# Optimization experiments

Measured on AMD Instinct MI355X. Metric: run time of the kernel, lower is better.

Reference implementation:

```python
import jax, jax.numpy as jnp
import numpy as np

VF = 3          # vote_factor
GRID = 0.1      # grid_size
P = 4           # padded per-group capacity (stands in for data-dependent max group size)
RATIO_MAX = 5   # original drops groups needing repeat ratio > 5
EPS = 1e-5
SHIFT, BASE = 512, 1024  # 3D->1D hash (int32-safe: BASE**3 < 2**31)


def _bn_relu(x, gamma, beta):
    # BatchNorm1d in train mode over the token (batch) axis; conv input is (N, C, 1)
    m = x.mean(axis=0)
    v = jnp.mean((x - m) ** 2, axis=0)  # biased variance, as torch BN uses for normalization
    return jax.nn.relu((x - m) * jax.lax.rsqrt(v + EPS) * gamma + beta)


def _one_sample(idv, cov, ftv, W1, b1, g1, be1, W2, b2, g2, be2, W3, b3):
    N, C = ftv.shape
    V = N * VF
    # conv1x1 stack == per-token linear layers
    h = _bn_relu(ftv @ W1.T + b1, g1, be1)
    h = _bn_relu(h @ W2.T + b2, g2, be2)
    log = (h @ W3.T + b3).reshape(N, VF, 3 + C)
    off3 = log[:, :, :3]                                  # (N, VF, 3)
    coor = (cov[:, None, :] + off3).reshape(V, 3)
    grid_res = (off3 / GRID).astype(jnp.int32)            # trunc toward zero, like .int()
    ind = (idv[:, None, :] + grid_res).reshape(V, 3)
    # Degenerate inner-dict loop (tensor keys hash by identity): every vote's feature
    # offset becomes offset[n][VF-1] * 3 / VF  (len(key)==3, idx stale at VF-1)
    feat_off = log[:, VF - 1, 3:] * (3.0 / VF)            # (N, C)
    feat = jnp.broadcast_to((ftv + feat_off)[:, None, :], (N, VF, C)).reshape(V, C)

    # group votes by quantized 3D index (tuple-key dict -> hash + unique + segment ops)
    hc = jnp.clip(ind, -SHIFT, SHIFT - 1) + SHIFT
    keys = (hc[:, 0] * BASE + hc[:, 1]) * BASE + hc[:, 2]  # (V,) int32
    _, inv = jnp.unique(keys, size=V, fill_value=-1, return_inverse=True)
    inv = inv.reshape(-1)
    ones = jnp.ones((V,), jnp.int32)
    counts = jax.ops.segment_sum(ones, inv, num_segments=V)          # group sizes
    order = jnp.argsort(inv)                                          # votes sorted by group
    starts = jnp.cumsum(counts) - counts
    first = jax.ops.segment_min(jnp.arange(V, dtype=jnp.int32), inv, num_segments=V)
    first = jnp.where(counts > 0, first, 0)
    ind_buf = jnp.where((counts > 0)[:, None], ind[first], 0).astype(jnp.int32)

    cnt_safe = jnp.maximum(counts, 1)
    p = jnp.arange(P, dtype=jnp.int32)
    src_pos = starts[:, None] + (p[None, :] % cnt_safe[:, None])      # (V, P) repeat-fill
    src = order[src_pos]
    valid = (counts > 0) & (counts * RATIO_MAX >= P)                  # ceil(P/cnt) <= 5
    coor_buf = jnp.where(valid[:, None, None], coor[src], 0.0)        # (V, P, 3)
    feat_buf = jnp.where(valid[:, None, None], feat[src], 0.0)        # (V, P, C)
    return ind_buf, coor_buf, feat_buf, valid


def setup_inputs() -> dict:
    key = jax.random.key(0)
    ks = jax.random.split(key, 12)
    B, N, C = 2, 16384, 128
    s = 1.0 / np.sqrt(C)
    return {
        "ID": jax.random.randint(ks[0], (B, N, 3), 0, 100, dtype=jnp.int32),
        "CO": jax.random.normal(ks[1], (B, N, 3), jnp.float32),
        "FT": jax.random.normal(ks[2], (B, N, C), jnp.float32),
        "W1": jax.random.normal(ks[3], (C, C), jnp.float32) * s,
        "b1": jnp.zeros((C,), jnp.float32),
        "g1": 1.0 + 0.1 * jax.random.normal(ks[4], (C,), jnp.float32),
        "be1": 0.1 * jax.random.normal(ks[5], (C,), jnp.float32),
        "W2": jax.random.normal(ks[6], (C, C), jnp.float32) * s,
        "b2": jnp.zeros((C,), jnp.float32),
        "g2": 1.0 + 0.1 * jax.random.normal(ks[7], (C,), jnp.float32),
        "be2": 0.1 * jax.random.normal(ks[8], (C,), jnp.float32),
        "W3": jax.random.normal(ks[9], ((3 + C) * VF, C), jnp.float32) * s,
        "b3": 0.01 * jax.random.normal(ks[10], ((3 + C) * VF,), jnp.float32),
    }


def reference(ID, CO, FT, W1, b1, g1, be1, W2, b2, g2, be2, W3, b3):
    outs = [_one_sample(ID[i], CO[i], FT[i], W1, b1, g1, be1, W2, b2, g2, be2, W3, b3)
            for i in range(ID.shape[0])]  # small fixed batch loop
    ind_buf = jnp.stack([o[0] for o in outs])
    coor_buf = jnp.stack([o[1] for o in outs])
    feat_buf = jnp.stack([o[2] for o in outs])
    mask = jnp.stack([o[3] for o in outs])
    return ind_buf, coor_buf, feat_buf, mask
```

## Files before the change

### kernel.cpp

```cpp
#include <hip/hip_runtime.h>

constexpr int Bn = 2;
constexpr int Nn = 16384;
constexpr int Cc = 128;
constexpr int Vv = Nn * 3;
constexpr int Pp = 4;
constexpr int SB = 48;
constexpr int HB = 96;

constexpr size_t IND0  = 0;
constexpr size_t COOR0 = (size_t)Bn * Vv * 3;
constexpr size_t FEAT0 = COOR0 + (size_t)Bn * Vv * Pp * 3;
constexpr size_t MASK0 = FEAT0 + (size_t)Bn * Vv * Pp * Cc;

__global__ __launch_bounds__(256) void gemm1(
    const float* __restrict__ A, const float* __restrict__ W,
    const float* __restrict__ bias, float* __restrict__ out,
    unsigned* __restrict__ HZ)
{
    __shared__ float As[64 * 36];
    __shared__ float Ws[128 * 36];

    int t = threadIdx.x;
    {
        int gid = blockIdx.x * 256 + t;
        if (gid < 3 * Bn * SB * 1024 / 4)
            ((uint4*)HZ)[gid] = make_uint4(0u, 0u, 0u, 0u);
    }

    int bid = blockIdx.x;
    int s = bid >> 8, rb = bid & 255;
    const float* Ag = A + (size_t)s * Nn * Cc + (size_t)rb * 64 * Cc;
    float* outg = out + (size_t)s * Nn * Cc + (size_t)rb * 64 * Cc;

    int tx = t & 15, ty = t >> 4;
    int arow = t >> 3, ac4 = (t & 7) * 4;

    float acc[4][8];
    #pragma unroll
    for (int i = 0; i < 4; ++i)
        #pragma unroll
        for (int j = 0; j < 8; ++j) acc[i][j] = 0.f;

    float4 aR[2], wR[4];
    #pragma unroll
    for (int r = 0; r < 2; ++r)
        aR[r] = *(const float4*)(Ag + (size_t)(arow + r * 32) * Cc + ac4);
    #pragma unroll
    for (int r = 0; r < 4; ++r)
        wR[r] = *(const float4*)(W + (size_t)(arow + r * 32) * Cc + ac4);

    for (int stage = 0; stage < 4; ++stage) {
        if (stage) __syncthreads();
        #pragma unroll
        for (int r = 0; r < 2; ++r)
            *(float4*)&As[(arow + r * 32) * 36 + ac4] = aR[r];
        #pragma unroll
        for (int r = 0; r < 4; ++r)
            *(float4*)&Ws[(arow + r * 32) * 36 + ac4] = wR[r];
        if (stage < 3) {
            int k1 = (stage + 1) * 32;
            #pragma unroll
            for (int r = 0; r < 2; ++r)
                aR[r] = *(const float4*)(Ag + (size_t)(arow + r * 32) * Cc + k1 + ac4);
            #pragma unroll
            for (int r = 0; r < 4; ++r)
                wR[r] = *(const float4*)(W + (size_t)(arow + r * 32) * Cc + k1 + ac4);
        }
        __syncthreads();
        #pragma unroll
        for (int k4 = 0; k4 < 8; ++k4) {
            int k = k4 * 4;
            float4 av[4];
            #pragma unroll
            for (int i = 0; i < 4; ++i) av[i] = *(const float4*)&As[(i * 16 + ty) * 36 + k];
            #pragma unroll
            for (int j = 0; j < 8; ++j) {
                float4 wv = *(const float4*)&Ws[(j * 16 + tx) * 36 + k];
                #pragma unroll
                for (int i = 0; i < 4; ++i) {
                    float a0 = acc[i][j];
                    a0 = fmaf(av[i].x, wv.x, a0);
                    a0 = fmaf(av[i].y, wv.y, a0);
                    a0 = fmaf(av[i].z, wv.z, a0);
                    a0 = fmaf(av[i].w, wv.w, a0);
                    acc[i][j] = a0;
                }
            }
        }
    }
    #pragma unroll
    for (int j = 0; j < 8; ++j) {
        int col = j * 16 + tx;
        float bv = bias[col];
        #pragma unroll
        for (int i = 0; i < 4; ++i)
            outg[(size_t)(i * 16 + ty) * Cc + col] = acc[i][j] + bv;
    }
}

__global__ __launch_bounds__(256) void gemm_t2(
    const float* __restrict__ A, const float* __restrict__ W,
    const float* __restrict__ bias, const float* __restrict__ part,
    const float* __restrict__ g, const float* __restrict__ be,
    float* __restrict__ out)
{
    __shared__ float As[64 * 36];
    __shared__ float Ws[128 * 36];
    __shared__ float ssl[2 * Cc];

    int t = threadIdx.x;
    int bid = blockIdx.x;
    int s = bid >> 8, rb = bid & 255;
    const float* Ag = A + (size_t)s * Nn * Cc + (size_t)rb * 64 * Cc;
    float* outg = out + (size_t)s * Nn * Cc + (size_t)rb * 64 * Cc;

    if (t < Cc) {
        const float* pp = part + (size_t)s * 64 * 2 * Cc;
        float sm = 0.f, sq = 0.f;
        #pragma unroll 8
        for (int b = 0; b < 64; ++b) {
            sm += pp[(size_t)b * 2 * Cc + t];
            sq += pp[(size_t)b * 2 * Cc + Cc + t];
        }
        float m   = sm / (float)Nn;
        float var = sq / (float)Nn - m * m;
        float inv = 1.0f / sqrtf(var + 1e-5f);
        float sc  = g[t] * inv;
        ssl[t]      = sc;
        ssl[Cc + t] = be[t] - m * sc;
    }
    __syncthreads();

    int tx = t & 15, ty = t >> 4;
    int arow = t >> 3, ac4 = (t & 7) * 4;

    float acc[4][8];
    #pragma unroll
    for (int i = 0; i < 4; ++i)
        #pragma unroll
        for (int j = 0; j < 8; ++j) acc[i][j] = 0.f;

    float4 aR[2], wR[4];
    #pragma unroll
    for (int r = 0; r < 2; ++r)
        aR[r] = *(const float4*)(Ag + (size_t)(arow + r * 32) * Cc + ac4);
    #pragma unroll
    for (int r = 0; r < 4; ++r)
        wR[r] = *(const float4*)(W + (size_t)(arow + r * 32) * Cc + ac4);

    for (int stage = 0; stage < 4; ++stage) {
        int k0 = stage * 32;
        if (stage) __syncthreads();
        #pragma unroll
        for (int r = 0; r < 2; ++r) {
            float4 v = aR[r];
            int ch = k0 + ac4;
            v.x = fmaxf(0.f, fmaf(v.x, ssl[ch + 0], ssl[Cc + ch + 0]));
            v.y = fmaxf(0.f, fmaf(v.y, ssl[ch + 1], ssl[Cc + ch + 1]));
            v.z = fmaxf(0.f, fmaf(v.z, ssl[ch + 2], ssl[Cc + ch + 2]));
            v.w = fmaxf(0.f, fmaf(v.w, ssl[ch + 3], ssl[Cc + ch + 3]));
            *(float4*)&As[(arow + r * 32) * 36 + ac4] = v;
        }
        #pragma unroll
        for (int r = 0; r < 4; ++r)
            *(float4*)&Ws[(arow + r * 32) * 36 + ac4] = wR[r];
        if (stage < 3) {
            int k1 = k0 + 32;
            #pragma unroll
            for (int r = 0; r < 2; ++r)
                aR[r] = *(const float4*)(Ag + (size_t)(arow + r * 32) * Cc + k1 + ac4);
            #pragma unroll
            for (int r = 0; r < 4; ++r)
                wR[r] = *(const float4*)(W + (size_t)(arow + r * 32) * Cc + k1 + ac4);
        }
        __syncthreads();
        #pragma unroll
        for (int k4 = 0; k4 < 8; ++k4) {
            int k = k4 * 4;
            float4 av[4];
            #pragma unroll
            for (int i = 0; i < 4; ++i) av[i] = *(const float4*)&As[(i * 16 + ty) * 36 + k];
            #pragma unroll
            for (int j = 0; j < 8; ++j) {
                float4 wv = *(const float4*)&Ws[(j * 16 + tx) * 36 + k];
                #pragma unroll
                for (int i = 0; i < 4; ++i) {
                    float a0 = acc[i][j];
                    a0 = fmaf(av[i].x, wv.x, a0);
                    a0 = fmaf(av[i].y, wv.y, a0);
                    a0 = fmaf(av[i].z, wv.z, a0);
                    a0 = fmaf(av[i].w, wv.w, a0);
                    acc[i][j] = a0;
                }
            }
        }
    }
    #pragma unroll
    for (int j = 0; j < 8; ++j) {
        int col = j * 16 + tx;
        float bv = bias[col];
        #pragma unroll
        for (int i = 0; i < 4; ++i)
            outg[(size_t)(i * 16 + ty) * Cc + col] = acc[i][j] + bv;
    }
}

__global__ __launch_bounds__(256) void gemm3_fused(
    const float* __restrict__ A, const float* __restrict__ W,
    const float* __restrict__ bias, const float* __restrict__ part,
    const float* __restrict__ g, const float* __restrict__ be,
    const float* __restrict__ FT, const float* __restrict__ CO,
    const int* __restrict__ ID,
    float* __restrict__ featb, float* __restrict__ coor,
    int* __restrict__ indb, unsigned* __restrict__ keys,
    unsigned* __restrict__ idx0, unsigned* __restrict__ hist0)
{
    __shared__ float As[64 * 36];
    __shared__ float Ws[144 * 36];
    __shared__ float ssl[2 * Cc];

    int bid = blockIdx.x;
    int s = bid >> 8, rb = bid & 255;
    const float* Ag = A + (size_t)s * Nn * Cc + (size_t)rb * 64 * Cc;

    int t = threadIdx.x, tx = t & 15, ty = t >> 4;

    if (t < Cc) {
        const float* pp = part + (size_t)s * 64 * 2 * Cc;
        float sm = 0.f, sq = 0.f;
        #pragma unroll 8
        for (int b = 0; b < 64; ++b) {
            sm += pp[(size_t)b * 2 * Cc + t];
            sq += pp[(size_t)b * 2 * Cc + Cc + t];
        }
        float m   = sm / (float)Nn;
        float var = sq / (float)Nn - m * m;
        float inv = 1.0f / sqrtf(var + 1e-5f);
        float sc  = g[t] * inv;
        ssl[t]      = sc;
        ssl[Cc + t] = be[t] - m * sc;
    }
    __syncthreads();

    float acc[4][9];
    #pragma unroll
    for (int i = 0; i < 4; ++i)
        #pragma unroll
        for (int j = 0; j < 9; ++j) acc[i][j] = 0.f;

    for (int stage = 0; stage < 4; ++stage) {
        int k0 = stage * 32;
        if (stage) __syncthreads();
        #pragma unroll
        for (int r = 0; r < 2; ++r) {
            int idx = r * 256 + t;
            int row = idx >> 3, c4 = (idx & 7) * 4;
            float4 v = *(const float4*)(Ag + (size_t)row * Cc + k0 + c4);
            int ch = k0 + c4;
            v.x = fmaxf(0.f, fmaf(v.x, ssl[ch + 0], ssl[Cc + ch + 0]));
            v.y = fmaxf(0.f, fmaf(v.y, ssl[ch + 1], ssl[Cc + ch + 1]));
            v.z = fmaxf(0.f, fmaf(v.z, ssl[ch + 2], ssl[Cc + ch + 2]));
            v.w = fmaxf(0.f, fmaf(v.w, ssl[ch + 3], ssl[Cc + ch + 3]));
            *(float4*)&As[row * 36 + c4] = v;
        }
        for (int idx = t; idx < 144 * 8; idx += 256) {
            int row = idx >> 3, c4 = (idx & 7) * 4;
            float4 v = make_float4(0.f, 0.f, 0.f, 0.f);
            if (row < 137) {
                int wr = (row < 9) ? (row / 3) * 131 + (row % 3) : row + 256;
                v = *(const float4*)(W + (size_t)wr * Cc + k0 + c4);
            }
            *(float4*)&Ws[row * 36 + c4] = v;
        }
        __syncthreads();
        #pragma unroll
        for (int k4 = 0; k4 < 8; ++k4) {
            int k = k4 * 4;
            float4 av[4];
            #pragma unroll
            for (int i = 0; i < 4; ++i) av[i] = *(const float4*)&As[(i * 16 + ty) * 36 + k];
            #pragma unroll
            for (int j = 0; j < 9; ++j) {
                float4 wv = *(const float4*)&Ws[(j * 16 + tx) * 36 + k];
                #pragma unroll
                for (int i = 0; i < 4; ++i) {
                    float a0 = acc[i][j];
                    a0 = fmaf(av[i].x, wv.x, a0);
                    a0 = fmaf(av[i].y, wv.y, a0);
                    a0 = fmaf(av[i].z, wv.z, a0);
                    a0 = fmaf(av[i].w, wv.w, a0);
                    acc[i][j] = a0;
                }
            }
        }
    }

    __syncthreads();
    __shared__ float L9[64 * 12];
    int n0 = rb * 64;
    const float* FTg = FT + ((size_t)s * Nn + n0) * Cc;
    float* FBg = featb + ((size_t)s * Nn + n0) * Cc;
    #pragma unroll
    for (int j = 0; j < 9; ++j) {
        int col = j * 16 + tx;
        if (col < 9) {
            float bv = bias[(col / 3) * 131 + col % 3];
            #pragma unroll
            for (int i = 0; i < 4; ++i)
                L9[(i * 16 + ty) * 12 + col] = acc[i][j] + bv;
        } else if (col < 137) {
            int ch = col - 9;
            float bv = bias[col + 256];
            #pragma unroll
            for (int i = 0; i < 4; ++i) {
                int row = i * 16 + ty;
                float lg = acc[i][j] + bv;
                FBg[(size_t)row * Cc + ch] = FTg[(size_t)row * Cc + ch] + lg;
            }
        }
    }
    __syncthreads();
    if (t < 192) {
        int row = t / 3, jv = t - row * 3;
        int n = n0 + row, v = n * 3 + jv;
        size_t vb = (size_t)s * Vv + v;
        float o0 = L9[row * 12 + jv * 3 + 0];
        float o1 = L9[row * 12 + jv * 3 + 1];
        float o2 = L9[row * 12 + jv * 3 + 2];
        const float* co = CO + ((size_t)s * Nn + n) * 3;
        coor[vb * 3 + 0] = co[0] + o0;
        coor[vb * 3 + 1] = co[1] + o1;
        coor[vb * 3 + 2] = co[2] + o2;
        const int* id = ID + ((size_t)s * Nn + n) * 3;
        int gi0 = (int)(o0 / 0.1f), gi1 = (int)(o1 / 0.1f), gi2 = (int)(o2 / 0.1f);
        int i0 = id[0] + gi0, i1 = id[1] + gi1, i2 = id[2] + gi2;
        indb[vb * 3 + 0] = i0; indb[vb * 3 + 1] = i1; indb[vb * 3 + 2] = i2;
        int h0 = min(max(i0, -512), 511) + 512;
        int h1 = min(max(i1, -512), 511) + 512;
        int h2 = min(max(i2, -512), 511) + 512;
        unsigned key = ((unsigned)h0 * 1024u + (unsigned)h1) * 1024u + (unsigned)h2;
        keys[vb] = key;
        idx0[vb] = (unsigned)v;
        atomicAdd(&hist0[(size_t)s * SB * 1024 + (size_t)(v >> 10) * 1024 + (key & 1023u)], 1u);
    }
}

__global__ void colstats(const float* __restrict__ Y, float* __restrict__ part)
{
    int blk = blockIdx.x;
    int s = blk >> 6, b = blk & 63;
    const float* Yp = Y + (size_t)s * Nn * Cc + (size_t)b * 256 * Cc;
    int c = threadIdx.x;
    float sm = 0.f, sq = 0.f;
    #pragma unroll 8
    for (int r = 0; r < 256; ++r) {
        float v = Yp[(size_t)r * Cc + c];
        sm += v; sq += v * v;
    }
    float* pp = part + ((size_t)s * 64 + b) * 2 * Cc;
    pp[c] = sm;
    pp[Cc + c] = sq;
}

template<int PASS>
__global__ __launch_bounds__(512) void scat(
    const unsigned* __restrict__ kIn, const unsigned* __restrict__ iIn,
    unsigned* __restrict__ kOut, unsigned* __restrict__ iOut,
    const unsigned* __restrict__ hist, unsigned* __restrict__ nextH)
{
    __shared__ unsigned hw[8 * 1024];
    __shared__ unsigned tot[1024];
    __shared__ unsigned wtot[8];
    int t = threadIdx.x, lane = t & 63, w = t >> 6;
    int blk = blockIdx.x, s = blk / SB, b = blk % SB;

    #pragma unroll
    for (int i = 0; i < 16; ++i) hw[w * 1024 + i * 64 + lane] = 0u;

    const uint2* hs2 = (const uint2*)(hist + (size_t)s * SB * 1024);
    int d0 = 2 * t, d1 = 2 * t + 1;
    unsigned run0 = 0, run1 = 0, my0 = 0, my1 = 0;
    #pragma unroll 4
    for (int bb = 0; bb < SB; ++bb) {
        uint2 v = hs2[bb * 512 + t];
        if (bb == b) { my0 = run0; my1 = run1; }
        run0 += v.x; run1 += v.y;
    }
    unsigned pair = run0 + run1;
    unsigned S = pair;
    #pragma unroll
    for (int o = 1; o < 64; o <<= 1) {
        unsigned v = __shfl_up(S, o);
        if (lane >= o) S += v;
    }
    unsigned pairExcl = S - pair;
    unsigned wTot = __shfl(S, 63);
    if (lane == 63) wtot[w] = S;
    __syncthreads();
    unsigned waveBase = 0;
    #pragma unroll
    for (int ww = 0; ww < 8; ++ww)
        if (ww < w) waveBase += wtot[ww];
    (void)wTot;
    tot[d0] = waveBase + pairExcl + my0;
    tot[d1] = waveBase + pairExcl + run0 + my1;

    size_t base = (size_t)s * Vv + (size_t)b * 1024;
    unsigned keyE[2], idxE[2], rkE[2], dE[2];
    #pragma unroll
    for (int e = 0; e < 2; ++e) {
        int pos = w * 128 + e * 64 + lane;
        keyE[e] = kIn[base + pos];
        idxE[e] = iIn[base + pos];
        unsigned d = (keyE[e] >> (PASS * 10)) & 1023u;
        dE[e] = d;
        unsigned long long m = ~0ull;
        #pragma unroll
        for (int bit = 0; bit < 10; ++bit) {
            bool bbit = (d >> bit) & 1u;
            unsigned long long bal = __ballot(bbit);
            m &= bbit ? bal : ~bal;
        }
        int lanesBelow = __popcll(m & ((1ull << lane) - 1ull));
        int cnt = __popcll(m);
        int leader = __ffsll((unsigned long long)m) - 1;
        unsigned basec = hw[w * 1024 + d];
        if (lane == leader) hw[w * 1024 + d] = basec + (unsigned)cnt;
        rkE[e] = basec + (unsigned)lanesBelow;
    }
    __syncthreads();
    {
        unsigned r0 = 0, r1 = 0;
        for (int ww = 0; ww < 8; ++ww) {
            unsigned v0 = hw[ww * 1024 + d0], v1 = hw[ww * 1024 + d1];
            hw[ww * 1024 + d0] = r0; hw[ww * 1024 + d1] = r1;
            r0 += v0; r1 += v1;
        }
    }
    __syncthreads();
    #pragma unroll
    for (int e = 0; e < 2; ++e) {
        unsigned dest = tot[dE[e]] + hw[w * 1024 + dE[e]] + rkE[e];
        kOut[(size_t)s * Vv + dest] = keyE[e];
        iOut[(size_t)s * Vv + dest] = idxE[e];
        if constexpr (PASS < 2) {
            unsigned d2 = (keyE[e] >> ((PASS + 1) * 10)) & 1023u;
            atomicAdd(&nextH[(size_t)s * SB * 1024 + (size_t)(dest >> 10) * 1024 + d2], 1u);
        }
    }
}

__global__ __launch_bounds__(512) void ranksall(const unsigned* __restrict__ skeys,
                                                unsigned* __restrict__ start,
                                                unsigned* __restrict__ nu)
{
    int blk = blockIdx.x;
    int s = blk / HB, cb = blk % HB;
    int t = threadIdx.x, lane = t & 63, w = t >> 6;
    size_t base = (size_t)s * Vv;

    __shared__ unsigned cnt[HB];
    __shared__ unsigned pre[HB + 1];
    __shared__ unsigned wsum[8];

    for (int cc = w * 12; cc < w * 12 + 12; ++cc) {
        unsigned tc = 0;
        #pragma unroll
        for (int sub = 0; sub < 8; ++sub) {
            int i = cc * 512 + sub * 64 + lane;
            unsigned k = skeys[base + i];
            bool head = (i == 0) || (skeys[base + i - 1] != k);
            tc += (unsigned)__popcll(__ballot(head));
        }
        if (lane == 0) cnt[cc] = tc;
    }
    __syncthreads();
    if (t == 0) {
        unsigned run = 0;
        for (int i = 0; i < HB; ++i) { pre[i] = run; run += cnt[i]; }
        pre[HB] = run;
    }
    __syncthreads();

    int i = cb * 512 + t;
    unsigned k = skeys[base + i];
    bool head = (i == 0) || (skeys[base + i - 1] != k);
    unsigned long long bal = __ballot(head);
    if (lane == 0) wsum[w] = (unsigned)__popcll(bal);
    __syncthreads();
    unsigned wbase = 0;
    for (int ww = 0; ww < w; ++ww) wbase += wsum[ww];
    unsigned lpre = (unsigned)__popcll(bal & ((1ull << lane) - 1ull));
    if (head)
        start[(size_t)s * (Vv + 1) + pre[cb] + wbase + lpre] = (unsigned)i;
    if (cb == 0 && t == 0) {
        nu[s] = pre[HB];
        start[(size_t)s * (Vv + 1) + pre[HB]] = (unsigned)Vv;
    }
}

__global__ __launch_bounds__(512) void outputk(
    const unsigned* __restrict__ sidx, const unsigned* __restrict__ start,
    const unsigned* __restrict__ nu, const int* __restrict__ indb,
    const float* __restrict__ coor, const float* __restrict__ featb,
    float* __restrict__ out)
{
    int wid = threadIdx.x >> 6, lane = threadIdx.x & 63;
    int g = blockIdx.x * 8 + wid;
    int s = g / Vv, u = g - s * Vv;
    size_t su = (size_t)s * Vv + u;
    bool valid = (unsigned)u < nu[s];
    float4* out4 = (float4*)out;
    int f = lane & 31, jlo = lane >> 5;
    if (valid) {
        const unsigned* st = start + (size_t)s * (Vv + 1);
        unsigned i0 = st[u], i1 = st[u + 1];
        unsigned c = i1 - i0;
        unsigned my = sidx[(size_t)s * Vv + i0 + ((unsigned)(lane & 3)) % c];
        unsigned sv[4];
        sv[0] = __shfl(my, 0); sv[1] = __shfl(my, 1);
        sv[2] = __shfl(my, 2); sv[3] = __shfl(my, 3);
        const float4* fb = (const float4*)(featb + (size_t)s * Nn * Cc);
        #pragma unroll
        for (int h = 0; h < 2; ++h) {
            int j = jlo + 2 * h;
            out4[(FEAT0 >> 2) + su * 128 + (size_t)j * 32 + f] =
                fb[(size_t)(sv[j] / 3) * 32 + f];
        }
        if (lane < 12)
            out[COOR0 + su * 12 + lane] =
                coor[((size_t)s * Vv + sv[lane / 3]) * 3 + lane % 3];
        else if (lane < 15)
            out[IND0 + su * 3 + (lane - 12)] =
                (float)indb[((size_t)s * Vv + sv[0]) * 3 + (lane - 12)];
        else if (lane == 15)
            out[MASK0 + su] = 1.f;
    } else {
        float4 z = make_float4(0.f, 0.f, 0.f, 0.f);
        #pragma unroll
        for (int h = 0; h < 2; ++h)
            out4[(FEAT0 >> 2) + su * 128 + (size_t)(jlo + 2 * h) * 32 + f] = z;
        if (lane < 12)       out[COOR0 + su * 12 + lane] = 0.f;
        else if (lane < 15)  out[IND0 + su * 3 + (lane - 12)] = 0.f;
        else if (lane == 15) out[MASK0 + su] = 0.f;
    }
}

extern "C" void kernel_launch(void* const* d_in, const int* in_sizes, int n_in,
                              void* d_out, int out_size, void* d_ws, size_t ws_size,
                              hipStream_t stream)
{
    const int*   ID  = (const int*)d_in[0];
    const float* CO  = (const float*)d_in[1];
    const float* FT  = (const float*)d_in[2];
    const float* W1  = (const float*)d_in[3];
    const float* b1  = (const float*)d_in[4];
    const float* g1  = (const float*)d_in[5];
    const float* be1 = (const float*)d_in[6];
    const float* W2  = (const float*)d_in[7];
    const float* b2  = (const float*)d_in[8];
    const float* g2  = (const float*)d_in[9];
    const float* be2 = (const float*)d_in[10];
    const float* W3  = (const float*)d_in[11];
    const float* b3  = (const float*)d_in[12];
    float* out = (float*)d_out;

    char* wsc = (char*)d_ws;
    size_t off = 0;
    auto alloc = [&](size_t elems) -> void* {
        void* p = wsc + off;
        off += ((elems * 4 + 255) & ~(size_t)255);
        return p;
    };
    float*    H1b   = (float*)alloc((size_t)Bn * Nn * Cc);
    float*    H2b   = (float*)alloc((size_t)Bn * Nn * Cc);
    float*    PART  = (float*)alloc((size_t)Bn * 64 * 2 * Cc);
    float*    COORb = (float*)alloc((size_t)Bn * Vv * 3);
    int*      INDB  = (int*)alloc((size_t)Bn * Vv * 3);
    float*    FEATB = (float*)alloc((size_t)Bn * Nn * Cc);
    unsigned* KA    = (unsigned*)alloc((size_t)Bn * Vv);
    unsigned* IA    = (unsigned*)alloc((size_t)Bn * Vv);
    unsigned* KB    = (unsigned*)alloc((size_t)Bn * Vv);
    unsigned* IB    = (unsigned*)alloc((size_t)Bn * Vv);
    unsigned* H0h   = (unsigned*)alloc((size_t)Bn * SB * 1024);
    unsigned* H1h   = (unsigned*)alloc((size_t)Bn * SB * 1024);
    unsigned* H2h   = (unsigned*)alloc((size_t)Bn * SB * 1024);
    unsigned* NUp   = (unsigned*)alloc((size_t)Bn);
    unsigned* STp   = (unsigned*)alloc((size_t)Bn * (Vv + 1));
    (void)in_sizes; (void)n_in; (void)out_size; (void)ws_size;

    gemm1<<<Bn * 256, 256, 0, stream>>>(FT, W1, b1, H1b, H0h);
    colstats<<<Bn * 64, 128, 0, stream>>>(H1b, PART);
    gemm_t2<<<Bn * 256, 256, 0, stream>>>(H1b, W2, b2, PART, g1, be1, H2b);
    colstats<<<Bn * 64, 128, 0, stream>>>(H2b, PART);
    gemm3_fused<<<Bn * 256, 256, 0, stream>>>(
        H2b, W3, b3, PART, g2, be2, FT, CO, ID, FEATB, COORb, INDB, KA, IA, H0h);
    scat<0><<<Bn * SB, 512, 0, stream>>>(KA, IA, KB, IB, H0h, H1h);
    scat<1><<<Bn * SB, 512, 0, stream>>>(KB, IB, KA, IA, H1h, H2h);
    scat<2><<<Bn * SB, 512, 0, stream>>>(KA, IA, KB, IB, H2h, nullptr);
    ranksall<<<Bn * HB, 512, 0, stream>>>(KB, STp, NUp);
    outputk<<<Bn * Vv / 8, 512, 0, stream>>>(IB, STp, NUp, INDB, COORb, FEATB, out);
}
```

Before: 228.7 us.

## Split head counting into separate kernel and shrink output block size

The per-block recount of all group heads inside ranksall is replaced by a separate headsct kernel that writes one head count per 512-element chunk, followed by ranksk, which prefix-sums those partials. This removes the redundant full-array scan each rank block did, at the cost of an extra kernel launch and a small global round trip. The output kernel goes from 512-thread to 256-thread blocks, still one wave per group, and two unroll pragmas plus an unused shuffle are dropped.

```diff
diff --git a/kernel.cpp b/kernel.cpp
--- a/kernel.cpp
+++ b/kernel.cpp
@@ -118,7 +118,6 @@
     if (t < Cc) {
         const float* pp = part + (size_t)s * 64 * 2 * Cc;
         float sm = 0.f, sq = 0.f;
-        #pragma unroll 8
         for (int b = 0; b < 64; ++b) {
             sm += pp[(size_t)b * 2 * Cc + t];
             sq += pp[(size_t)b * 2 * Cc + Cc + t];
@@ -229,7 +228,6 @@
     if (t < Cc) {
         const float* pp = part + (size_t)s * 64 * 2 * Cc;
         float sm = 0.f, sq = 0.f;
-        #pragma unroll 8
         for (int b = 0; b < 64; ++b) {
             sm += pp[(size_t)b * 2 * Cc + t];
             sq += pp[(size_t)b * 2 * Cc + Cc + t];
@@ -395,14 +393,12 @@
         if (lane >= o) S += v;
     }
     unsigned pairExcl = S - pair;
-    unsigned wTot = __shfl(S, 63);
     if (lane == 63) wtot[w] = S;
     __syncthreads();
     unsigned waveBase = 0;
     #pragma unroll
     for (int ww = 0; ww < 8; ++ww)
         if (ww < w) waveBase += wtot[ww];
-    (void)wTot;
     tot[d0] = waveBase + pairExcl + my0;
     tot[d1] = waveBase + pairExcl + run0 + my1;
 
@@ -451,63 +447,73 @@
     }
 }
 
-__global__ __launch_bounds__(512) void ranksall(const unsigned* __restrict__ skeys,
-                                                unsigned* __restrict__ start,
-                                                unsigned* __restrict__ nu)
+__global__ __launch_bounds__(512) void headsct(const unsigned* __restrict__ skeys,
+                                               unsigned* __restrict__ hpart)
 {
     int blk = blockIdx.x;
-    int s = blk / HB, cb = blk % HB;
-    int t = threadIdx.x, lane = t & 63, w = t >> 6;
+    int s = blk / HB, b = blk % HB;
+    int i = b * 512 + threadIdx.x;
     size_t base = (size_t)s * Vv;
-
-    __shared__ unsigned cnt[HB];
+    unsigned k = skeys[base + i];
+    bool head = (i == 0) || (skeys[base + i - 1] != k);
+    __shared__ unsigned wsum[8];
+    unsigned long long bal = __ballot(head);
+    int lane = threadIdx.x & 63, wid = threadIdx.x >> 6;
+    if (lane == 0) wsum[wid] = (unsigned)__popcll(bal);
+    __syncthreads();
+    if (threadIdx.x == 0) {
+        unsigned tot = 0;
+        for (int w = 0; w < 8; ++w) tot += wsum[w];
+        hpart[s * HB + b] = tot;
+    }
+}
+
+__global__ __launch_bounds__(512) void ranksk(const unsigned* __restrict__ skeys,
+                                              const unsigned* __restrict__ hpart,
+                                              unsigned* __restrict__ start,
+                                              unsigned* __restrict__ nu)
+{
+    int blk = blockIdx.x;
+    int s = blk / HB, b = blk % HB;
+    int t = threadIdx.x;
+    __shared__ unsigned hp[HB];
     __shared__ unsigned pre[HB + 1];
-    __shared__ unsigned wsum[8];
-
-    for (int cc = w * 12; cc < w * 12 + 12; ++cc) {
-        unsigned tc = 0;
-        #pragma unroll
-        for (int sub = 0; sub < 8; ++sub) {
-            int i = cc * 512 + sub * 64 + lane;
-            unsigned k = skeys[base + i];
-            bool head = (i == 0) || (skeys[base + i - 1] != k);
-            tc += (unsigned)__popcll(__ballot(head));
-        }
-        if (lane == 0) cnt[cc] = tc;
-    }
+    if (t < HB) hp[t] = hpart[s * HB + t];
     __syncthreads();
     if (t == 0) {
         unsigned run = 0;
-        for (int i = 0; i < HB; ++i) { pre[i] = run; run += cnt[i]; }
+        for (int i = 0; i < HB; ++i) { pre[i] = run; run += hp[i]; }
         pre[HB] = run;
     }
     __syncthreads();
-
-    int i = cb * 512 + t;
+    int i = b * 512 + t;
+    size_t base = (size_t)s * Vv;
     unsigned k = skeys[base + i];
     bool head = (i == 0) || (skeys[base + i - 1] != k);
     unsigned long long bal = __ballot(head);
-    if (lane == 0) wsum[w] = (unsigned)__popcll(bal);
+    int lane = t & 63, wid = t >> 6;
+    __shared__ unsigned wsum[8];
+    if (lane == 0) wsum[wid] = (unsigned)__popcll(bal);
     __syncthreads();
     unsigned wbase = 0;
-    for (int ww = 0; ww < w; ++ww) wbase += wsum[ww];
+    for (int w = 0; w < wid; ++w) wbase += wsum[w];
     unsigned lpre = (unsigned)__popcll(bal & ((1ull << lane) - 1ull));
     if (head)
-        start[(size_t)s * (Vv + 1) + pre[cb] + wbase + lpre] = (unsigned)i;
-    if (cb == 0 && t == 0) {
+        start[(size_t)s * (Vv + 1) + pre[b] + wbase + lpre] = (unsigned)i;
+    if (b == 0 && t == 0) {
         nu[s] = pre[HB];
         start[(size_t)s * (Vv + 1) + pre[HB]] = (unsigned)Vv;
     }
 }
 
-__global__ __launch_bounds__(512) void outputk(
+__global__ __launch_bounds__(256) void outputk(
     const unsigned* __restrict__ sidx, const unsigned* __restrict__ start,
     const unsigned* __restrict__ nu, const int* __restrict__ indb,
     const float* __restrict__ coor, const float* __restrict__ featb,
     float* __restrict__ out)
 {
     int wid = threadIdx.x >> 6, lane = threadIdx.x & 63;
-    int g = blockIdx.x * 8 + wid;
+    int g = blockIdx.x * 4 + wid;
     int s = g / Vv, u = g - s * Vv;
     size_t su = (size_t)s * Vv + u;
     bool valid = (unsigned)u < nu[s];
@@ -586,6 +592,7 @@
     unsigned* H0h   = (unsigned*)alloc((size_t)Bn * SB * 1024);
     unsigned* H1h   = (unsigned*)alloc((size_t)Bn * SB * 1024);
     unsigned* H2h   = (unsigned*)alloc((size_t)Bn * SB * 1024);
+    unsigned* HP    = (unsigned*)alloc((size_t)Bn * HB);
     unsigned* NUp   = (unsigned*)alloc((size_t)Bn);
     unsigned* STp   = (unsigned*)alloc((size_t)Bn * (Vv + 1));
     (void)in_sizes; (void)n_in; (void)out_size; (void)ws_size;
@@ -599,6 +606,7 @@
     scat<0><<<Bn * SB, 512, 0, stream>>>(KA, IA, KB, IB, H0h, H1h);
     scat<1><<<Bn * SB, 512, 0, stream>>>(KB, IB, KA, IA, H1h, H2h);
     scat<2><<<Bn * SB, 512, 0, stream>>>(KA, IA, KB, IB, H2h, nullptr);
-    ranksall<<<Bn * HB, 512, 0, stream>>>(KB, STp, NUp);
-    outputk<<<Bn * Vv / 8, 512, 0, stream>>>(IB, STp, NUp, INDB, COORb, FEATB, out);
-}
+    headsct<<<Bn * HB, 512, 0, stream>>>(KB, HP);
+    ranksk<<<Bn * HB, 512, 0, stream>>>(KB, HP, STp, NUp);
+    outputk<<<Bn * Vv / 4, 256, 0, stream>>>(IB, STp, NUp, INDB, COORb, FEATB, out);
+}
```

New measurement: 224.1 us. -2.0%, faster.
